# Kernel optimization log

Measured on AMD Instinct MI355X. Metric: run time of the kernel, lower is better.

Reference implementation:

```python
import jax, jax.numpy as jnp
import numpy as np

E = 80000   # number of directed edges
T = 80000   # number of triplets
HID = 256   # hidden_channels
INT = 64    # int_emb_size == num_bilinear
NR = 6      # num_radial
NS = 7      # num_spherical
BD = 8      # basis_emb_size_dist
BA = 8      # basis_emb_size_angle


def swish(x):
    return x * jax.nn.sigmoid(x)


def setup_inputs() -> dict:
    key = jax.random.key(0)
    ks = jax.random.split(key, 16)
    inp = {
        "x1": jax.random.normal(ks[0], (E, HID), dtype=jnp.float32),
        "rbf0": jax.random.normal(ks[1], (E, NR), dtype=jnp.float32),
        "sbf": jax.random.normal(ks[2], (T, NS * NR), dtype=jnp.float32),
        "t": jax.random.normal(ks[3], (T, NS * NS * NR), dtype=jnp.float32),
        "x_kj": jax.random.normal(ks[4], (E, HID), dtype=jnp.float32),
        "x_ji": jax.random.normal(ks[5], (E, HID), dtype=jnp.float32),
        "idx_kj": jax.random.randint(ks[6], (T,), 0, E, dtype=jnp.int32),
        "idx_ji": jax.random.randint(ks[7], (T,), 0, E, dtype=jnp.int32),
        # weights stored [in, out] so y = x @ W (torch Linear uses weight.T)
        "W_rbf1": jax.random.normal(ks[8], (NR, BD), dtype=jnp.float32) * 0.3,
        "W_rbf2": jax.random.normal(ks[9], (BD, HID), dtype=jnp.float32) * 0.3,
        "W_sbf1": jax.random.normal(ks[10], (NS * NR, BA), dtype=jnp.float32) * 0.15,
        "W_sbf2": jax.random.normal(ks[11], (BA, INT), dtype=jnp.float32) * 0.3,
        "W_t1": jax.random.normal(ks[12], (NS * NS * NR, INT), dtype=jnp.float32) * 0.06,
        "W_down": jax.random.normal(ks[13], (HID, INT), dtype=jnp.float32) * 0.06,
        "W_up": jax.random.normal(ks[14], (INT, HID), dtype=jnp.float32) * 0.12,
        # bilinear weight W: [int_emb, num_bilinear, int_emb], std = 2/int_emb
        "W_bil": jax.random.normal(ks[15], (INT, INT, INT), dtype=jnp.float32) * (2.0 / INT),
    }
    return inp


def reference(x1, rbf0, sbf, t, x_kj, x_ji, idx_kj, idx_ji,
              W_rbf1, W_rbf2, W_sbf1, W_sbf2, W_t1, W_down, W_up, W_bil):
    # rbf projection: [E, NR] -> [E, HID]
    rbf = (rbf0 @ W_rbf1) @ W_rbf2
    xk = x_kj * rbf                          # [E, HID]
    xk = swish(xk @ W_down)                  # [E, INT]
    # sbf projection: [T, NS*NR] -> [T, INT]
    s = (sbf @ W_sbf1) @ W_sbf2
    xk = xk[idx_kj] * s                      # gather to triplets: [T, INT]
    tt = t @ W_t1                            # [T, INT] (num_bilinear dim)
    # bilinear: 'wj,wl,ijl->wi' with W_bil [INT(i), INT(j), INT(l)]
    a = jnp.einsum('wj,ijl->wil', tt, W_bil)  # [T, INT, INT]
    out_t = jnp.einsum('wil,wl->wi', a, xk)   # [T, INT]
    # scatter-add triplets back to edges
    agg = jax.ops.segment_sum(out_t, idx_ji, num_segments=x1.shape[0])  # [E, INT]
    return swish(agg @ W_up)                  # [E, HID]
```

## Files before the change

kernel.cpp:

```cpp
#include <hip/hip_runtime.h>
#include <hip/hip_fp16.h>

#define E_N 80000
#define T_N 80000
#define NB1 313

typedef _Float16 h4 __attribute__((ext_vector_type(4)));
typedef _Float16 h8 __attribute__((ext_vector_type(8)));
typedef float    f4 __attribute__((ext_vector_type(4)));
typedef float    f2 __attribute__((ext_vector_type(2)));

static __device__ __forceinline__ float swishf(float x) {
    return x / (1.0f + __expf(-x));
}

static __device__ __forceinline__ void pack_w_dev(const float* __restrict__ src,
                                                  h8* __restrict__ dst,
                                                  int g, int Ksrc, int N, int NT) {
    int lane = g & 63, frag = g >> 6;
    int nt = frag % NT, kt = frag / NT;
    int quad = (lane >> 4);
    int n = nt * 16 + (lane & 15);
    int k0 = kt * 32 + quad * 8;
    h8 v;
#pragma unroll
    for (int u = 0; u < 8; ++u) {
        int k = k0 + u;
        v[u] = (k < Ksrc) ? (_Float16)src[(size_t)k * N + n] : (_Float16)0.0f;
    }
    dst[g] = v;
}

__global__ __launch_bounds__(256) void kpack_all(const float* __restrict__ Wb,  h8* __restrict__ wbil,
                                                 const float* __restrict__ Wd,  h8* __restrict__ wpd,
                                                 const float* __restrict__ Wt,  h8* __restrict__ wpt,
                                                 const float* __restrict__ Wu,  h8* __restrict__ wpu) {
    int b = blockIdx.x, tid = threadIdx.x;
    if (b < 128) {
        int g = b * 256 + tid;
        int i    = ((g >> 6) & 3) * 16 + (g & 15);
        int c    = (g >> 8) & 1;
        int j    = g >> 9;
        int quad = (g >> 4) & 3;
        int l0   = c * 32 + quad * 8;
        const float* src = Wb + ((i * 64 + j) << 6) + l0;
        h8 v;
#pragma unroll
        for (int u = 0; u < 8; ++u) v[u] = (_Float16)src[u];
        wbil[g] = v;
    } else if (b < 136) {
        pack_w_dev(Wd, wpd, (b - 128) * 256 + tid, 256, 64, 4);
    } else if (b < 146) {
        pack_w_dev(Wt, wpt, (b - 136) * 256 + tid, 294, 64, 4);
    } else {
        pack_w_dev(Wu, wpu, (b - 146) * 256 + tid, 64, 256, 16);
    }
}

__global__ __launch_bounds__(256, 4) void k1_down(const float* __restrict__ rbf0,
                                                  const float* __restrict__ xkj,
                                                  const float* __restrict__ W_rbf1,
                                                  const float* __restrict__ W_rbf2,
                                                  const h8* __restrict__ wpd,
                                                  _Float16* __restrict__ xke) {
    int tid = threadIdx.x;
    int lane = tid & 63, wv = tid >> 6;
    int m = lane & 15, quad = lane >> 4;
    int rowb = blockIdx.x * 128 + wv * 32;

    float r8[2][8];
#pragma unroll
    for (int rt = 0; rt < 2; ++rt) {
        int r = rowb + rt * 16 + m;
        float rv[6];
#pragma unroll
        for (int q = 0; q < 6; ++q) rv[q] = rbf0[(size_t)r * 6 + q];
#pragma unroll
        for (int p = 0; p < 8; ++p) {
            float s = 0.f;
#pragma unroll
            for (int q = 0; q < 6; ++q) s += rv[q] * W_rbf1[q * 8 + p];
            r8[rt][p] = s;
        }
    }

    f4 acc[2][4] = {};
#pragma unroll
    for (int kb = 0; kb < 8; ++kb) {
        int k0 = kb * 32 + quad * 8;
        h8 afrag[2];
#pragma unroll
        for (int rt = 0; rt < 2; ++rt) {
            f4 rlo = {}, rhi = {};
#pragma unroll
            for (int p = 0; p < 8; ++p) {
                rlo += r8[rt][p] * *(const f4*)(W_rbf2 + p * 256 + k0);
                rhi += r8[rt][p] * *(const f4*)(W_rbf2 + p * 256 + k0 + 4);
            }
            size_t base = (size_t)(rowb + rt * 16 + m) * 256 + k0;
            f4 xlo = *(const f4*)(xkj + base);
            f4 xhi = *(const f4*)(xkj + base + 4);
            rlo *= xlo; rhi *= xhi;
            h8 a;
#pragma unroll
            for (int u = 0; u < 4; ++u) {
                a[u]     = (_Float16)rlo[u];
                a[u + 4] = (_Float16)rhi[u];
            }
            afrag[rt] = a;
        }
#pragma unroll
        for (int nt = 0; nt < 4; ++nt) {
            h8 b = wpd[((kb * 4 + nt) << 6) + lane];
            acc[0][nt] = __builtin_amdgcn_mfma_f32_16x16x32_f16(afrag[0], b, acc[0][nt], 0, 0, 0);
            acc[1][nt] = __builtin_amdgcn_mfma_f32_16x16x32_f16(afrag[1], b, acc[1][nt], 0, 0, 0);
        }
    }

#pragma unroll
    for (int rt = 0; rt < 2; ++rt)
#pragma unroll
        for (int nt = 0; nt < 4; ++nt)
#pragma unroll
            for (int rr = 0; rr < 4; ++rr) {
                int row = rowb + rt * 16 + quad * 4 + rr;
                xke[(size_t)row * 64 + nt * 16 + m] = (_Float16)swishf(acc[rt][nt][rr]);
            }
}

__global__ __launch_bounds__(256) void kb1_tproj(const float* __restrict__ tin,
                                                 const h8* __restrict__ wpt,
                                                 _Float16* __restrict__ ttb) {
    int tid = threadIdx.x;
    int lane = tid & 63, wv = tid >> 6;
    int m = lane & 15, quad = lane >> 4;
    int rowb = blockIdx.x * 128 + wv * 32;

    f4 acc[2][4] = {};
    for (int ktg = 0; ktg < 10; ++ktg) {
        int k0 = ktg * 32 + quad * 8;
        h8 afrag[2];
#pragma unroll
        for (int rt = 0; rt < 2; ++rt) {
            size_t base = (size_t)(rowb + rt * 16 + m) * 294 + k0;
            h8 a;
            if (k0 + 8 <= 294) {
                f2 t0 = *(const f2*)(tin + base);
                f2 t1 = *(const f2*)(tin + base + 2);
                f2 t2 = *(const f2*)(tin + base + 4);
                f2 t3 = *(const f2*)(tin + base + 6);
                a[0] = (_Float16)t0[0]; a[1] = (_Float16)t0[1];
                a[2] = (_Float16)t1[0]; a[3] = (_Float16)t1[1];
                a[4] = (_Float16)t2[0]; a[5] = (_Float16)t2[1];
                a[6] = (_Float16)t3[0]; a[7] = (_Float16)t3[1];
            } else {
#pragma unroll
                for (int u = 0; u < 8; ++u) {
                    int k = k0 + u;
                    a[u] = (k < 294) ? (_Float16)tin[base + u] : (_Float16)0.0f;
                }
            }
            afrag[rt] = a;
        }
#pragma unroll
        for (int nt = 0; nt < 4; ++nt) {
            h8 b = wpt[((ktg * 4 + nt) << 6) + lane];
#pragma unroll
            for (int rt = 0; rt < 2; ++rt)
                acc[rt][nt] = __builtin_amdgcn_mfma_f32_16x16x32_f16(afrag[rt], b, acc[rt][nt], 0, 0, 0);
        }
    }

#pragma unroll
    for (int rt = 0; rt < 2; ++rt)
#pragma unroll
        for (int nt = 0; nt < 4; ++nt)
#pragma unroll
            for (int rr = 0; rr < 4; ++rr) {
                int row = rowb + rt * 16 + quad * 4 + rr;
                ttb[(size_t)row * 64 + nt * 16 + m] = (_Float16)acc[rt][nt][rr];
            }
}

__global__ __launch_bounds__(256) void kb2_gather(const float* __restrict__ sbf,
                                                  const float* __restrict__ W_sbf1,
                                                  const float* __restrict__ W_sbf2,
                                                  const _Float16* __restrict__ xke,
                                                  const int* __restrict__ idx_kj,
                                                  const int* __restrict__ idx_ji,
                                                  int* __restrict__ hist,
                                                  _Float16* __restrict__ xkt) {
    __shared__ float sbfL[32 * 42];
    __shared__ float midL[32 * 8];
    int tid = threadIdx.x;
    int row0 = blockIdx.x * 32;
    if (tid < 32) atomicAdd(&hist[idx_ji[row0 + tid]], 1);
    for (int i = tid; i < 32 * 42; i += 256)
        sbfL[i] = sbf[(size_t)row0 * 42 + i];
    __syncthreads();
    {
        int r = tid >> 3, p = tid & 7;
        float mm = 0.f;
#pragma unroll
        for (int q = 0; q < 42; ++q) mm += sbfL[r * 42 + q] * W_sbf1[q * 8 + p];
        midL[r * 8 + p] = mm;
    }
    __syncthreads();
    int r = tid >> 3;
    int c0 = (tid & 7) * 8;
    int w = row0 + r;
    int e = idx_kj[w];
    f4 sa = {}, sb = {};
#pragma unroll
    for (int p = 0; p < 8; ++p) {
        float mm = midL[r * 8 + p];
        sa += mm * *(const f4*)(W_sbf2 + (p << 6) + c0);
        sb += mm * *(const f4*)(W_sbf2 + (p << 6) + c0 + 4);
    }
    h8 xv = *(const h8*)(xke + (size_t)e * 64 + c0);
    h8 o;
#pragma unroll
    for (int u = 0; u < 4; ++u) {
        o[u]     = (_Float16)((float)xv[u]     * sa[u]);
        o[u + 4] = (_Float16)((float)xv[u + 4] * sb[u]);
    }
    *(h8*)(xkt + (size_t)w * 64 + c0) = o;
}

__global__ __launch_bounds__(256) void kscan1(const int* __restrict__ hist, int* __restrict__ bsum) {
    int t = threadIdx.x;
    int w = blockIdx.x * 256 + t;
    int v = (w < E_N) ? hist[w] : 0;
#pragma unroll
    for (int off = 32; off; off >>= 1) v += __shfl_down(v, off, 64);
    __shared__ int ls[4];
    if ((t & 63) == 0) ls[t >> 6] = v;
    __syncthreads();
    if (t == 0) bsum[blockIdx.x] = ls[0] + ls[1] + ls[2] + ls[3];
}

__global__ __launch_bounds__(512) void kscan2(const int* __restrict__ bsum, int* __restrict__ boff) {
    __shared__ int s[512];
    int t = threadIdx.x;
    int v = (t < NB1) ? bsum[t] : 0;
    s[t] = v;
    __syncthreads();
    for (int off = 1; off < 512; off <<= 1) {
        int x = (t >= off) ? s[t - off] : 0;
        __syncthreads();
        s[t] += x;
        __syncthreads();
    }
    if (t < NB1) boff[t] = s[t] - v;
}

__global__ __launch_bounds__(256) void kscan3(const int* __restrict__ hist, const int* __restrict__ boff,
                                              int* __restrict__ start, int* __restrict__ nxt) {
    __shared__ int s[256];
    int t = threadIdx.x;
    int w = blockIdx.x * 256 + t;
    int v = (w < E_N) ? hist[w] : 0;
    s[t] = v;
    __syncthreads();
    for (int off = 1; off < 256; off <<= 1) {
        int x = (t >= off) ? s[t - off] : 0;
        __syncthreads();
        s[t] += x;
        __syncthreads();
    }
    if (w < E_N) {
        int st = boff[blockIdx.x] + s[t] - v;
        start[w] = st;
        nxt[w]   = st;
    }
}

__global__ __launch_bounds__(256) void kfill(const int* __restrict__ idx_ji,
                                             int* __restrict__ nxt, int* __restrict__ pos) {
    int w = blockIdx.x * 256 + threadIdx.x;
    if (w < T_N) pos[w] = atomicAdd(&nxt[idx_ji[w]], 1);
}

__global__ __launch_bounds__(128, 3) void kb3_bilinear(const _Float16* __restrict__ xkt,
                                                       const _Float16* __restrict__ ttp,
                                                       const h8* __restrict__ wpack,
                                                       const int* __restrict__ pos,
                                                       float* __restrict__ outp) {
    int tid = threadIdx.x;
    int lane = tid & 63, wv = tid >> 6;
    int qrow = lane & 15, quad = lane >> 4;
    int row0 = blockIdx.x * 128 + wv * 64;
    int jlo = blockIdx.y * 32;

    h8 xa[4][2];
#pragma unroll
    for (int rt = 0; rt < 4; ++rt) {
        const _Float16* rp = xkt + (size_t)(row0 + rt * 16 + qrow) * 64 + quad * 8;
        xa[rt][0] = *(const h8*)rp;
        xa[rt][1] = *(const h8*)(rp + 32);
    }

    f4 acc[4][4] = {};
#pragma unroll
    for (int jg = 0; jg < 4; ++jg) {
        h8 tg[4];
#pragma unroll
        for (int rt = 0; rt < 4; ++rt)
            tg[rt] = *(const h8*)(ttp + (size_t)(row0 + rt * 16 + qrow) * 64 + jlo + jg * 8);
#pragma unroll
        for (int ju = 0; ju < 8; ++ju) {
            int j = jlo + jg * 8 + ju;
            const h8* wj = wpack + (((size_t)j * 8) << 6) + lane;
            h8 b0[4], b1[4];
#pragma unroll
            for (int nt = 0; nt < 4; ++nt) {
                b0[nt] = wj[nt << 6];
                b1[nt] = wj[(4 + nt) << 6];
            }
#pragma unroll
            for (int rt = 0; rt < 4; ++rt) {
                _Float16 tv = tg[rt][ju];
                h8 t8 = {tv, tv, tv, tv, tv, tv, tv, tv};
                h8 a0 = xa[rt][0] * t8;
                h8 a1 = xa[rt][1] * t8;
#pragma unroll
                for (int nt = 0; nt < 4; ++nt) {
                    acc[rt][nt] = __builtin_amdgcn_mfma_f32_16x16x32_f16(a0, b0[nt], acc[rt][nt], 0, 0, 0);
                    acc[rt][nt] = __builtin_amdgcn_mfma_f32_16x16x32_f16(a1, b1[nt], acc[rt][nt], 0, 0, 0);
                }
            }
        }
    }

    float* __restrict__ outh = outp + (size_t)blockIdx.y * ((size_t)T_N * 64);
#pragma unroll
    for (int rt = 0; rt < 4; ++rt) {
#pragma unroll
        for (int rr = 0; rr < 4; ++rr) {
            int w = row0 + rt * 16 + quad * 4 + rr;
            float* dst = outh + (size_t)pos[w] * 64 + qrow;
#pragma unroll
            for (int nt = 0; nt < 4; ++nt)
                dst[nt * 16] = acc[rt][nt][rr];
        }
    }
}

__global__ __launch_bounds__(256) void kagg(const float* __restrict__ outp,
                                            const int* __restrict__ start,
                                            const int* __restrict__ nxt,
                                            float* __restrict__ agg) {
    int tid = threadIdx.x;
    int e = blockIdx.x * 16 + (tid >> 4);
    int c4 = (tid & 15) * 4;
    int p0 = start[e], p1 = nxt[e];
    const float* o1 = outp + (size_t)T_N * 64;
    f4 s = {0.f, 0.f, 0.f, 0.f};
    for (int p = p0; p < p1; ++p) {
        s += *(const f4*)(outp + (size_t)p * 64 + c4);
        s += *(const f4*)(o1   + (size_t)p * 64 + c4);
    }
    *(f4*)(agg + (size_t)e * 64 + c4) = s;
}

__global__ __launch_bounds__(256) void k4_up(const float* __restrict__ agg,
                                             const h8* __restrict__ wpu,
                                             float* __restrict__ out) {
    int tid = threadIdx.x;
    int lane = tid & 63, wv = tid >> 6;
    int m = lane & 15, quad = lane >> 4;
    int rowb = blockIdx.x * 64 + wv * 16;

    f4 acc[16] = {};
#pragma unroll
    for (int kt = 0; kt < 2; ++kt) {
        const float* ap = agg + (size_t)(rowb + m) * 64 + kt * 32 + quad * 8;
        f4 alo = *(const f4*)ap;
        f4 ahi = *(const f4*)(ap + 4);
        h8 a;
#pragma unroll
        for (int u = 0; u < 4; ++u) {
            a[u]     = (_Float16)alo[u];
            a[u + 4] = (_Float16)ahi[u];
        }
#pragma unroll
        for (int nt = 0; nt < 16; ++nt) {
            h8 b = wpu[((kt * 16 + nt) << 6) + lane];
            acc[nt] = __builtin_amdgcn_mfma_f32_16x16x32_f16(a, b, acc[nt], 0, 0, 0);
        }
    }

#pragma unroll
    for (int nt = 0; nt < 16; ++nt)
#pragma unroll
        for (int rr = 0; rr < 4; ++rr) {
            int row = rowb + quad * 4 + rr;
            out[(size_t)row * 256 + nt * 16 + m] = swishf(acc[nt][rr]);
        }
}

extern "C" void kernel_launch(void* const* d_in, const int* in_sizes, int n_in,
                              void* d_out, int out_size, void* d_ws, size_t ws_size,
                              hipStream_t stream) {
    const float* rbf0   = (const float*)d_in[1];
    const float* sbf    = (const float*)d_in[2];
    const float* tin    = (const float*)d_in[3];
    const float* xkj    = (const float*)d_in[4];
    const int*   idx_kj = (const int*)d_in[6];
    const int*   idx_ji = (const int*)d_in[7];
    const float* W_rbf1 = (const float*)d_in[8];
    const float* W_rbf2 = (const float*)d_in[9];
    const float* W_sbf1 = (const float*)d_in[10];
    const float* W_sbf2 = (const float*)d_in[11];
    const float* W_t1   = (const float*)d_in[12];
    const float* W_down = (const float*)d_in[13];
    const float* W_up   = (const float*)d_in[14];
    const float* W_bil  = (const float*)d_in[15];

    char* ws = (char*)d_ws;
    _Float16* xke = (_Float16*)ws;
    float*    agg = (float*)(ws + 10240000);
    h8* wpack_bil = (h8*)(ws + 30720000);
    h8* wpd       = (h8*)(ws + 31244288);
    h8* wpt       = (h8*)(ws + 31277056);
    h8* wpu       = (h8*)(ws + 31318016);

    char* ob = (char*)d_out;
    _Float16* ttb  = (_Float16*)ob;
    _Float16* xkt  = (_Float16*)(ob + 10240000);
    float*    outp = (float*)(ob + 20480000);
    int* hist  = (int*)(ob + 61440000);
    int* start = (int*)(ob + 61760000);
    int* nxt   = (int*)(ob + 62080000);
    int* pos   = (int*)(ob + 62400000);
    int* bsum  = (int*)(ob + 62720000);
    int* boff  = (int*)(ob + 62724096);
    float* out = (float*)d_out;

    hipMemsetAsync(hist, 0, E_N * 4, stream);
    kpack_all<<<154, 256, 0, stream>>>(W_bil, wpack_bil, W_down, wpd, W_t1, wpt, W_up, wpu);
    k1_down<<<625, 256, 0, stream>>>(rbf0, xkj, W_rbf1, W_rbf2, wpd, xke);
    kb1_tproj<<<625, 256, 0, stream>>>(tin, wpt, ttb);
    kb2_gather<<<2500, 256, 0, stream>>>(sbf, W_sbf1, W_sbf2, xke, idx_kj, idx_ji, hist, xkt);
    kscan1<<<NB1, 256, 0, stream>>>(hist, bsum);
    kscan2<<<1, 512, 0, stream>>>(bsum, boff);
    kscan3<<<NB1, 256, 0, stream>>>(hist, boff, start, nxt);
    kfill<<<NB1, 256, 0, stream>>>(idx_ji, nxt, pos);
    kb3_bilinear<<<dim3(625, 2), 128, 0, stream>>>(xkt, ttb, wpack_bil, pos, outp);
    kagg<<<5000, 256, 0, stream>>>(outp, start, nxt, agg);
    k4_up<<<1250, 256, 0, stream>>>(agg, wpu, out);
}
```

Measured before the change: 474.6 us.

## Fuse segment aggregation into up-projection and software-pipeline bilinear weight loads

Measured after the change: 468.0 us. Within noise of the previous version (-1.4%).

```diff
diff --git a/kernel.cpp b/kernel.cpp
--- a/kernel.cpp
+++ b/kernel.cpp
@@ -300,34 +300,58 @@
         xa[rt][1] = *(const h8*)(rp + 32);
     }
 
+    const h8* wl = wpack + lane;
+
+    h8 bc[2][4];
+#pragma unroll
+    for (int nt = 0; nt < 4; ++nt)
+        bc[0][nt] = wl[((size_t)jlo * 8 + nt) << 6];
+
+    h8 tg[2][4];
+#pragma unroll
+    for (int rt = 0; rt < 4; ++rt)
+        tg[0][rt] = *(const h8*)(ttp + (size_t)(row0 + rt * 16 + qrow) * 64 + jlo);
+
     f4 acc[4][4] = {};
 #pragma unroll
     for (int jg = 0; jg < 4; ++jg) {
-        h8 tg[4];
-#pragma unroll
-        for (int rt = 0; rt < 4; ++rt)
-            tg[rt] = *(const h8*)(ttp + (size_t)(row0 + rt * 16 + qrow) * 64 + jlo + jg * 8);
+        const int tp = jg & 1;
+        if (jg < 3) {
+#pragma unroll
+            for (int rt = 0; rt < 4; ++rt)
+                tg[tp ^ 1][rt] = *(const h8*)(ttp + (size_t)(row0 + rt * 16 + qrow) * 64 + jlo + (jg + 1) * 8);
+        }
 #pragma unroll
         for (int ju = 0; ju < 8; ++ju) {
-            int j = jlo + jg * 8 + ju;
-            const h8* wj = wpack + (((size_t)j * 8) << 6) + lane;
-            h8 b0[4], b1[4];
-#pragma unroll
-            for (int nt = 0; nt < 4; ++nt) {
-                b0[nt] = wj[nt << 6];
-                b1[nt] = wj[(4 + nt) << 6];
-            }
+            const int u = jg * 8 + ju;
+            const int j = jlo + u;
+
+#pragma unroll
+            for (int nt = 0; nt < 4; ++nt)
+                bc[1][nt] = wl[((size_t)j * 8 + 4 + nt) << 6];
 #pragma unroll
             for (int rt = 0; rt < 4; ++rt) {
-                _Float16 tv = tg[rt][ju];
+                _Float16 tv = tg[tp][rt][ju];
                 h8 t8 = {tv, tv, tv, tv, tv, tv, tv, tv};
                 h8 a0 = xa[rt][0] * t8;
+#pragma unroll
+                for (int nt = 0; nt < 4; ++nt)
+                    acc[rt][nt] = __builtin_amdgcn_mfma_f32_16x16x32_f16(a0, bc[0][nt], acc[rt][nt], 0, 0, 0);
+            }
+
+            if (u < 31) {
+#pragma unroll
+                for (int nt = 0; nt < 4; ++nt)
+                    bc[0][nt] = wl[((size_t)(j + 1) * 8 + nt) << 6];
+            }
+#pragma unroll
+            for (int rt = 0; rt < 4; ++rt) {
+                _Float16 tv = tg[tp][rt][ju];
+                h8 t8 = {tv, tv, tv, tv, tv, tv, tv, tv};
                 h8 a1 = xa[rt][1] * t8;
 #pragma unroll
-                for (int nt = 0; nt < 4; ++nt) {
-                    acc[rt][nt] = __builtin_amdgcn_mfma_f32_16x16x32_f16(a0, b0[nt], acc[rt][nt], 0, 0, 0);
-                    acc[rt][nt] = __builtin_amdgcn_mfma_f32_16x16x32_f16(a1, b1[nt], acc[rt][nt], 0, 0, 0);
-                }
+                for (int nt = 0; nt < 4; ++nt)
+                    acc[rt][nt] = __builtin_amdgcn_mfma_f32_16x16x32_f16(a1, bc[1][nt], acc[rt][nt], 0, 0, 0);
             }
         }
     }
@@ -341,7 +365,7 @@
             float* dst = outh + (size_t)pos[w] * 64 + qrow;
 #pragma unroll
             for (int nt = 0; nt < 4; ++nt)
-                dst[nt * 16] = acc[rt][nt][rr];
+                __builtin_nontemporal_store(acc[rt][nt][rr], dst + nt * 16);
         }
     }
 }
@@ -363,9 +387,64 @@
     *(f4*)(agg + (size_t)e * 64 + c4) = s;
 }
 
-__global__ __launch_bounds__(256) void k4_up(const float* __restrict__ agg,
-                                             const h8* __restrict__ wpu,
-                                             float* __restrict__ out) {
+__global__ __launch_bounds__(256) void k4_up_fused(const float* __restrict__ outp,
+                                                   const int* __restrict__ start,
+                                                   const int* __restrict__ nxt,
+                                                   const h8* __restrict__ wpu,
+                                                   float* __restrict__ out) {
+    int tid = threadIdx.x;
+    int lane = tid & 63, wv = tid >> 6;
+    int m = lane & 15, quad = lane >> 4;
+    int rowb = blockIdx.x * 64 + wv * 16;
+    int row = rowb + m;
+
+    int p0 = start[row], p1 = nxt[row];
+    const float* o1 = outp + (size_t)T_N * 64;
+    f4 s0a = {}, s0b = {}, s1a = {}, s1b = {};
+    for (int p = p0; p < p1; ++p) {
+        const float* pr = outp + (size_t)p * 64 + quad * 8;
+        s0a += *(const f4*)(pr);
+        s0b += *(const f4*)(pr + 4);
+        s1a += *(const f4*)(pr + 32);
+        s1b += *(const f4*)(pr + 36);
+        const float* qr = o1 + (size_t)p * 64 + quad * 8;
+        s0a += *(const f4*)(qr);
+        s0b += *(const f4*)(qr + 4);
+        s1a += *(const f4*)(qr + 32);
+        s1b += *(const f4*)(qr + 36);
+    }
+
+    f4 acc[16] = {};
+#pragma unroll
+    for (int kt = 0; kt < 2; ++kt) {
+        f4 alo = kt ? s1a : s0a;
+        f4 ahi = kt ? s1b : s0b;
+        h8 a;
+#pragma unroll
+        for (int u = 0; u < 4; ++u) {
+            a[u]     = (_Float16)alo[u];
+            a[u + 4] = (_Float16)ahi[u];
+        }
+#pragma unroll
+        for (int nt = 0; nt < 16; ++nt) {
+            h8 b = wpu[((kt * 16 + nt) << 6) + lane];
+            acc[nt] = __builtin_amdgcn_mfma_f32_16x16x32_f16(a, b, acc[nt], 0, 0, 0);
+        }
+    }
+
+#pragma unroll
+    for (int nt = 0; nt < 16; ++nt)
+#pragma unroll
+        for (int rr = 0; rr < 4; ++rr) {
+            int orow = rowb + quad * 4 + rr;
+            __builtin_nontemporal_store(swishf(acc[nt][rr]),
+                                        out + (size_t)orow * 256 + nt * 16 + m);
+        }
+}
+
+__global__ __launch_bounds__(256) void k4_up_agg(const float* __restrict__ agg,
+                                                 const h8* __restrict__ wpu,
+                                                 float* __restrict__ out) {
     int tid = threadIdx.x;
     int lane = tid & 63, wv = tid >> 6;
     int m = lane & 15, quad = lane >> 4;
@@ -395,7 +474,8 @@
 #pragma unroll
         for (int rr = 0; rr < 4; ++rr) {
             int row = rowb + quad * 4 + rr;
-            out[(size_t)row * 256 + nt * 16 + m] = swishf(acc[nt][rr]);
+            __builtin_nontemporal_store(swishf(acc[nt][rr]),
+                                        out + (size_t)row * 256 + nt * 16 + m);
         }
 }
 
@@ -418,35 +498,66 @@
     const float* W_bil  = (const float*)d_in[15];
 
     char* ws = (char*)d_ws;
-    _Float16* xke = (_Float16*)ws;
-    float*    agg = (float*)(ws + 10240000);
-    h8* wpack_bil = (h8*)(ws + 30720000);
-    h8* wpd       = (h8*)(ws + 31244288);
-    h8* wpt       = (h8*)(ws + 31277056);
-    h8* wpu       = (h8*)(ws + 31318016);
-
     char* ob = (char*)d_out;
-    _Float16* ttb  = (_Float16*)ob;
-    _Float16* xkt  = (_Float16*)(ob + 10240000);
-    float*    outp = (float*)(ob + 20480000);
-    int* hist  = (int*)(ob + 61440000);
-    int* start = (int*)(ob + 61760000);
-    int* nxt   = (int*)(ob + 62080000);
-    int* pos   = (int*)(ob + 62400000);
-    int* bsum  = (int*)(ob + 62720000);
-    int* boff  = (int*)(ob + 62724096);
     float* out = (float*)d_out;
 
-    hipMemsetAsync(hist, 0, E_N * 4, stream);
-    kpack_all<<<154, 256, 0, stream>>>(W_bil, wpack_bil, W_down, wpd, W_t1, wpt, W_up, wpu);
-    k1_down<<<625, 256, 0, stream>>>(rbf0, xkj, W_rbf1, W_rbf2, wpd, xke);
-    kb1_tproj<<<625, 256, 0, stream>>>(tin, wpt, ttb);
-    kb2_gather<<<2500, 256, 0, stream>>>(sbf, W_sbf1, W_sbf2, xke, idx_kj, idx_ji, hist, xkt);
-    kscan1<<<NB1, 256, 0, stream>>>(hist, bsum);
-    kscan2<<<1, 512, 0, stream>>>(bsum, boff);
-    kscan3<<<NB1, 256, 0, stream>>>(hist, boff, start, nxt);
-    kfill<<<NB1, 256, 0, stream>>>(idx_ji, nxt, pos);
-    kb3_bilinear<<<dim3(625, 2), 128, 0, stream>>>(xkt, ttb, wpack_bil, pos, outp);
-    kagg<<<5000, 256, 0, stream>>>(outp, start, nxt, agg);
-    k4_up<<<1250, 256, 0, stream>>>(agg, wpu, out);
-}
+    const size_t WS_NEED_FUSED = 53120000;
+
+    if (ws_size >= WS_NEED_FUSED) {
+        _Float16* xke = (_Float16*)ws;
+        h8* wpack_bil = (h8*)(ws + 10240000);
+        h8* wpd       = (h8*)(ws + 10764288);
+        h8* wpt       = (h8*)(ws + 10797056);
+        h8* wpu       = (h8*)(ws + 10838016);
+        float* outp   = (float*)(ws + 10871808);
+        int* hist  = (int*)(ws + 51831808);
+        int* start = (int*)(ws + 52151808);
+        int* nxt   = (int*)(ws + 52471808);
+        int* pos   = (int*)(ws + 52791808);
+        int* bsum  = (int*)(ws + 53111808);
+        int* boff  = (int*)(ws + 53115904);
+        _Float16* ttb = (_Float16*)ob;
+        _Float16* xkt = (_Float16*)(ob + 10240000);
+
+        hipMemsetAsync(hist, 0, E_N * 4, stream);
+        kpack_all<<<154, 256, 0, stream>>>(W_bil, wpack_bil, W_down, wpd, W_t1, wpt, W_up, wpu);
+        k1_down<<<625, 256, 0, stream>>>(rbf0, xkj, W_rbf1, W_rbf2, wpd, xke);
+        kb1_tproj<<<625, 256, 0, stream>>>(tin, wpt, ttb);
+        kb2_gather<<<2500, 256, 0, stream>>>(sbf, W_sbf1, W_sbf2, xke, idx_kj, idx_ji, hist, xkt);
+        kscan1<<<NB1, 256, 0, stream>>>(hist, bsum);
+        kscan2<<<1, 512, 0, stream>>>(bsum, boff);
+        kscan3<<<NB1, 256, 0, stream>>>(hist, boff, start, nxt);
+        kfill<<<NB1, 256, 0, stream>>>(idx_ji, nxt, pos);
+        kb3_bilinear<<<dim3(625, 2), 128, 0, stream>>>(xkt, ttb, wpack_bil, pos, outp);
+        k4_up_fused<<<1250, 256, 0, stream>>>(outp, start, nxt, wpu, out);
+    } else {
+        _Float16* xke = (_Float16*)ws;
+        float*    agg = (float*)(ws + 10240000);
+        h8* wpack_bil = (h8*)(ws + 30720000);
+        h8* wpd       = (h8*)(ws + 31244288);
+        h8* wpt       = (h8*)(ws + 31277056);
+        h8* wpu       = (h8*)(ws + 31318016);
+        _Float16* ttb  = (_Float16*)ob;
+        _Float16* xkt  = (_Float16*)(ob + 10240000);
+        float*    outp = (float*)(ob + 20480000);
+        int* hist  = (int*)(ob + 61440000);
+        int* start = (int*)(ob + 61760000);
+        int* nxt   = (int*)(ob + 62080000);
+        int* pos   = (int*)(ob + 62400000);
+        int* bsum  = (int*)(ob + 62720000);
+        int* boff  = (int*)(ob + 62724096);
+
+        hipMemsetAsync(hist, 0, E_N * 4, stream);
+        kpack_all<<<154, 256, 0, stream>>>(W_bil, wpack_bil, W_down, wpd, W_t1, wpt, W_up, wpu);
+        k1_down<<<625, 256, 0, stream>>>(rbf0, xkj, W_rbf1, W_rbf2, wpd, xke);
+        kb1_tproj<<<625, 256, 0, stream>>>(tin, wpt, ttb);
+        kb2_gather<<<2500, 256, 0, stream>>>(sbf, W_sbf1, W_sbf2, xke, idx_kj, idx_ji, hist, xkt);
+        kscan1<<<NB1, 256, 0, stream>>>(hist, bsum);
+        kscan2<<<1, 512, 0, stream>>>(bsum, boff);
+        kscan3<<<NB1, 256, 0, stream>>>(hist, boff, start, nxt);
+        kfill<<<NB1, 256, 0, stream>>>(idx_ji, nxt, pos);
+        kb3_bilinear<<<dim3(625, 2), 128, 0, stream>>>(xkt, ttb, wpack_bil, pos, outp);
+        kagg<<<5000, 256, 0, stream>>>(outp, start, nxt, agg);
+        k4_up_agg<<<1250, 256, 0, stream>>>(agg, wpu, out);
+    }
+}
```
